# Optimization experiments

Measured on AMD Instinct MI355X. Metric: run time of the kernel, lower is better.

## Reference

```python
import jax, jax.numpy as jnp
import numpy as np

HIDDEN = 256
HORIZON = 24
FMET = 16
OUT = 1
EPS = 1e-5


def setup_inputs() -> dict:
    key = jax.random.key(0)
    ks = jax.random.split(key, 12)
    B, N = 16, 1000
    final_h = jax.random.normal(ks[0], (B, N, HIDDEN), dtype=jnp.float32)
    future_met = jax.random.normal(ks[1], (B, HORIZON, N, FMET), dtype=jnp.float32)
    # step_queries: xavier_uniform over (max_horizon, hidden)
    lim_q = float(np.sqrt(6.0 / (HORIZON + HIDDEN)))
    step_queries = jax.random.uniform(ks[2], (HORIZON, HIDDEN), minval=-lim_q, maxval=lim_q, dtype=jnp.float32)
    # future_met_proj: Linear(FMET -> HIDDEN); store weight as (FMET, HIDDEN)
    lim_fm = float(np.sqrt(1.0 / FMET))
    W_fm = jax.random.uniform(ks[3], (FMET, HIDDEN), minval=-lim_fm, maxval=lim_fm, dtype=jnp.float32)
    b_fm = jax.random.uniform(ks[4], (HIDDEN,), minval=-lim_fm, maxval=lim_fm, dtype=jnp.float32)
    gamma = jnp.ones((HIDDEN,), dtype=jnp.float32)
    beta = jnp.zeros((HIDDEN,), dtype=jnp.float32)
    lim1 = float(np.sqrt(1.0 / HIDDEN))
    W1 = jax.random.uniform(ks[5], (HIDDEN, HIDDEN), minval=-lim1, maxval=lim1, dtype=jnp.float32)
    b1 = jax.random.uniform(ks[6], (HIDDEN,), minval=-lim1, maxval=lim1, dtype=jnp.float32)
    W2 = jax.random.uniform(ks[7], (HIDDEN, OUT), minval=-lim1, maxval=lim1, dtype=jnp.float32)
    b2 = jax.random.uniform(ks[8], (OUT,), minval=-lim1, maxval=lim1, dtype=jnp.float32)
    return {
        "final_h": final_h,
        "future_met": future_met,
        "step_queries": step_queries,
        "W_fm": W_fm,
        "b_fm": b_fm,
        "gamma": gamma,
        "beta": beta,
        "W1": W1,
        "b1": b1,
        "W2": W2,
        "b2": b2,
    }


def _layer_norm(x, gamma, beta):
    mu = jnp.mean(x, axis=-1, keepdims=True)
    var = jnp.mean(jnp.square(x - mu), axis=-1, keepdims=True)
    return (x - mu) * jax.lax.rsqrt(var + EPS) * gamma + beta


def reference(final_h, future_met, step_queries, W_fm, b_fm, gamma, beta, W1, b1, W2, b2):
    # final_h: (B, N, H); future_met: (B, T, N, F)
    # combined: (B, N, T, H) = broadcast(final_h) + queries + proj(future_met)
    combined = final_h[:, :, None, :] + step_queries[None, None, :, :]
    fm = jnp.transpose(future_met, (0, 2, 1, 3))  # (B, N, T, F)
    combined = combined + (jnp.einsum("bntf,fh->bnth", fm, W_fm) + b_fm)
    x = _layer_norm(combined, gamma, beta)
    x = jax.nn.gelu(x @ W1 + b1, approximate=False)
    # dropout is identity in eval mode
    out = x @ W2 + b2  # (B, N, T, OUT)
    return jnp.transpose(out, (0, 2, 1, 3))  # (B, T, N, OUT)
```

## Files before the change

### kernel.cpp

```cpp
#include <hip/hip_runtime.h>
#include <hip/hip_bf16.h>
#include <stdint.h>

#define MROWS 32
#define LDA   264
#define FMS   40

typedef __bf16 bf16x8 __attribute__((ext_vector_type(8)));
typedef float  f32x4  __attribute__((ext_vector_type(4)));
typedef float  f32x2  __attribute__((ext_vector_type(2)));

__device__ __forceinline__ unsigned short f2bf(float f) {
    union { float f; uint32_t u; } v; v.f = f;
    return (unsigned short)((v.u + 0x7FFFu + ((v.u >> 16) & 1u)) >> 16);
}

__device__ __forceinline__ ushort2 pk_bf16(float a, float b) {
    union { __hip_bfloat162 v; ushort2 u; } c;
    c.v = __float22bfloat162_rn(make_float2(a, b));
    return c.u;
}

template <int CTRL>
__device__ __forceinline__ float dpp_radd(float x) {
    union { float f; int i; } a, b;
    a.f = x;
    b.i = __builtin_amdgcn_update_dpp(0, a.i, CTRL, 0xF, 0xF, true);
    return x + b.f;
}
#define ROW_SHR1 0x111
#define ROW_SHR2 0x112
#define ROW_SHR4 0x114
#define ROW_SHR8 0x118
__device__ __forceinline__ float dpp_rowsum(float x) {
    x = dpp_radd<ROW_SHR1>(x);
    x = dpp_radd<ROW_SHR2>(x);
    x = dpp_radd<ROW_SHR4>(x);
    x = dpp_radd<ROW_SHR8>(x);
    return x;
}

__device__ __forceinline__ f32x2 gelu_fast2(f32x2 v) {
    const f32x2 t = v * v;
    f32x2 p = t * 0.044715f + 1.0f;
    const f32x2 u = v * p;
    f32x2 e;
    e.x = __builtin_amdgcn_exp2f(u.x * -2.3021131160186336f);
    e.y = __builtin_amdgcn_exp2f(u.y * -2.3021131160186336f);
    f32x2 r;
    r.x = __builtin_amdgcn_rcpf(1.0f + e.x);
    r.y = __builtin_amdgcn_rcpf(1.0f + e.y);
    return v * r;
}

__device__ __forceinline__ int frag_n(int f) {
    return (f & 0xC0) | ((f & 3) << 4) | ((f >> 2) & 15);
}

__global__ __launch_bounds__(256) void prep1(const float* __restrict__ W1,
                                             const float* __restrict__ step_q,
                                             const float* __restrict__ b_fm,
                                             const float* __restrict__ W_fm,
                                             const float* __restrict__ gamma,
                                             const float* __restrict__ beta,
                                             unsigned short* __restrict__ w1frag,
                                             float* __restrict__ sqb,
                                             unsigned short* __restrict__ wfmfrag,
                                             float* __restrict__ gpart,
                                             float* __restrict__ bpart) {
    const int blk = blockIdx.x, tid = threadIdx.x;
    if (blk < 8) {
        __shared__ unsigned short T[256][40];
        const int kk = blk;
        float sg = 0.f, sb = 0.f;
        #pragma unroll
        for (int r = 0; r < 32; ++r) {
            const int k = (kk << 5) + r;
            const float wv = W1[k * 256 + tid];
            sg = fmaf(gamma[k], wv, sg);
            sb = fmaf(beta[k],  wv, sb);
            T[tid][r] = f2bf(wv);
        }
        gpart[(kk << 8) + tid] = sg;
        bpart[(kk << 8) + tid] = sb;
        __syncthreads();
        #pragma unroll
        for (int f = 0; f < 4; ++f) {
            const int fi = (f << 8) + tid;
            const int l = fi & 63, j = (fi >> 6) & 3, w = fi >> 8;
            const int n = (w << 6) + (j << 4) + (l & 15);
            const uint4 v = *(const uint4*)&T[n][(l >> 4) << 3];
            *(uint4*)&w1frag[((w << 5) + (j << 3) + kk) * 512 + (l << 3)] = v;
        }
    } else if (blk < 32) {
        const int t = blk - 8;
        const int n = frag_n(tid);
        sqb[t * 256 + tid] = step_q[t * 256 + n] + b_fm[n];
    } else {
        const int f  = blk - 32;
        const int fr = (f << 8) + tid;
        const int l = fr & 63, j = (fr >> 6) & 3, w = fr >> 8;
        const int n = (w << 6) + (j << 4) + (l & 15);
        const int qr = l >> 4;
        #pragma unroll
        for (int e = 0; e < 8; ++e) {
            const int k = (qr << 3) + e;
            wfmfrag[(fr << 3) + e] = (k < 16) ? f2bf(W_fm[(k << 8) + n]) : (unsigned short)0;
        }
    }
}

__global__ __launch_bounds__(256) void prep2(const float* __restrict__ gpart,
                                             const float* __restrict__ bpart,
                                             const float* __restrict__ b1,
                                             const float* __restrict__ W2,
                                             const float* __restrict__ gamma,
                                             float* __restrict__ gw1f,
                                             float* __restrict__ b1tf,
                                             float* __restrict__ w2f,
                                             float* __restrict__ gamf) {
    const int tid = threadIdx.x;
    const int n = frag_n(tid);
    float sg = 0.f, sb = 0.f;
    #pragma unroll
    for (int kk = 0; kk < 8; ++kk) {
        sg += gpart[(kk << 8) + n];
        sb += bpart[(kk << 8) + n];
    }
    gw1f[tid] = sg;
    b1tf[tid] = sb + b1[n];
    w2f[tid]  = W2[n];
    gamf[tid] = gamma[n];
}

__global__ __launch_bounds__(256, 6) void fused_head(
    const float* __restrict__ final_h, const float* __restrict__ future_met,
    const float* __restrict__ b2,      const unsigned short* __restrict__ w1frag,
    const float* __restrict__ sqb,     const unsigned short* __restrict__ wfmfrag,
    const float* __restrict__ gw1f,    const float* __restrict__ b1tf,
    const float* __restrict__ w2f,     const float* __restrict__ gamf,
    float* __restrict__ out)
{
    __shared__ __align__(16) unsigned short Abuf[MROWS * LDA];
    __shared__ __align__(16) unsigned short fmA[MROWS * FMS];
    __shared__ float2 red[4][MROWS];
    __shared__ float2 mv[MROWS];
    __shared__ float  part[4][MROWS];

    const int tid = threadIdx.x;
    const int w   = tid >> 6;
    const int l   = tid & 63;
    const int col = l & 15;
    const int qr  = l >> 4;
    const int m0  = blockIdx.x * MROWS;
    const int bn0 = m0 / 24;
    const int tt0 = m0 - bn0 * 24;
    const int fb  = (w << 6) + (col << 2);

    if (tid < 128) {
        const int row = tid >> 2, f0 = (tid & 3) << 2;
        const int tta = tt0 + row;
        const int sub = (tta >= 24) + (tta >= 48);
        const int tt  = tta - sub * 24;
        const int bn  = bn0 + sub;
        const int b   = bn / 1000, n = bn - b * 1000;
        const float4 v = *(const float4*)&future_met[((((b * 24 + tt) * 1000) + n) << 4) + f0];
        ushort2 lo = pk_bf16(v.x, v.y), hi = pk_bf16(v.z, v.w);
        ushort4 o; o.x = lo.x; o.y = lo.y; o.z = hi.x; o.w = hi.y;
        *(ushort4*)&fmA[row * FMS + f0] = o;
    }
    {
        const int row = tid >> 3, k = 16 + ((tid & 7) << 1);
        *(unsigned int*)&fmA[row * FMS + k] = 0u;
    }
    __syncthreads();

    const float4 g4 = *(const float4*)&gamf[fb];
    const f32x2 gA2 = {g4.x, g4.y}, gB2 = {g4.z, g4.w};

    const int dlo = qr << 2;
    const int slo = ((tt0 + dlo) >= 24) + ((tt0 + dlo) >= 48);
    const int shi = ((tt0 + dlo + 19) >= 24) + ((tt0 + dlo + 19) >= 48);
    float flo[4], fhi[4];
    {
        const float* fhl = final_h + ((bn0 + slo) << 8) + (w << 6) + col;
        const float* fhh = final_h + ((bn0 + shi) << 8) + (w << 6) + col;
        #pragma unroll
        for (int j = 0; j < 4; ++j) { flo[j] = fhl[j << 4]; fhi[j] = fhh[j << 4]; }
    }

    f32x4 acc[2][4];
    #pragma unroll
    for (int i = 0; i < 2; ++i) {
        #pragma unroll
        for (int r = 0; r < 4; ++r) {
            const int d   = (i << 4) + (qr << 2) + r;
            const int tta = tt0 + d;
            const int sub = (tta >= 24) + (tta >= 48);
            const int tt  = tta - sub * 24;
            const bool lo = (sub == slo);
            const float4 sb4 = *(const float4*)&sqb[(tt << 8) + fb];
            acc[i][0][r] = (lo ? flo[0] : fhi[0]) + sb4.x;
            acc[i][1][r] = (lo ? flo[1] : fhi[1]) + sb4.y;
            acc[i][2][r] = (lo ? flo[2] : fhi[2]) + sb4.z;
            acc[i][3][r] = (lo ? flo[3] : fhi[3]) + sb4.w;
        }
    }
    {
        const bf16x8 af0 = *(const bf16x8*)&fmA[col * FMS + (qr << 3)];
        const bf16x8 af1 = *(const bf16x8*)&fmA[(16 + col) * FMS + (qr << 3)];
        const unsigned short* Bwf = wfmfrag + (w << 11) + (l << 3);
        #pragma unroll
        for (int j = 0; j < 4; ++j) {
            const bf16x8 bf = *(const bf16x8*)(Bwf + (j << 9));
            acc[0][j] = __builtin_amdgcn_mfma_f32_16x16x32_bf16(af0, bf, acc[0][j], 0, 0, 0);
            acc[1][j] = __builtin_amdgcn_mfma_f32_16x16x32_bf16(af1, bf, acc[1][j], 0, 0, 0);
        }
    }

    #pragma unroll
    for (int i = 0; i < 2; ++i) {
        #pragma unroll
        for (int r = 0; r < 4; ++r) {
            const int m = (i << 4) + (qr << 2) + r;
            const f32x2 vA = {acc[i][0][r], acc[i][1][r]};
            const f32x2 vB = {acc[i][2][r], acc[i][3][r]};
            const f32x2 sv = vA + vB;
            const f32x2 qv = vA * vA + vB * vB;
            float s = sv.x + sv.y;
            float q = qv.x + qv.y;
            const f32x2 vjA = vA * gA2;
            const f32x2 vjB = vB * gB2;
            s = dpp_rowsum(s);
            q = dpp_rowsum(q);
            if (col == 15) red[w][m] = make_float2(s, q);
            const ushort2 p01 = pk_bf16(vjA.x, vjA.y);
            const ushort2 p23 = pk_bf16(vjB.x, vjB.y);
            unsigned short* Ab = &Abuf[m * LDA + (w << 6) + col];
            Ab[0]  = p01.x; Ab[16] = p01.y;
            Ab[32] = p23.x; Ab[48] = p23.y;
        }
    }
    __syncthreads();

    if (tid < MROWS) {
        const float2 a0 = red[0][tid], a1 = red[1][tid], a2 = red[2][tid], a3 = red[3][tid];
        const float S = a0.x + a1.x + a2.x + a3.x;
        const float Q = a0.y + a1.y + a2.y + a3.y;
        const float mu = S * 0.00390625f;
        const float rstd = rsqrtf(Q * 0.00390625f - mu * mu + 1e-5f);
        mv[tid] = make_float2(mu, rstd);
    }

    #pragma unroll
    for (int i = 0; i < 2; ++i)
        #pragma unroll
        for (int j = 0; j < 4; ++j)
            acc[i][j] = (f32x4){0.f, 0.f, 0.f, 0.f};

    {
        const unsigned short* Bw  = w1frag + (w << 14) + (l << 3);
        const unsigned short* Ab0 = &Abuf[col * LDA + (qr << 3)];
        const unsigned short* Ab1 = &Abuf[(16 + col) * LDA + (qr << 3)];
        #pragma unroll
        for (int kk = 0; kk < 8; ++kk) {
            const bf16x8 a0 = *(const bf16x8*)(Ab0 + (kk << 5));
            const bf16x8 a1 = *(const bf16x8*)(Ab1 + (kk << 5));
            #pragma unroll
            for (int j = 0; j < 4; ++j) {
                const bf16x8 bf = *(const bf16x8*)(Bw + (j << 12) + (kk << 9));
                acc[0][j] = __builtin_amdgcn_mfma_f32_16x16x32_bf16(a0, bf, acc[0][j], 0, 0, 0);
                acc[1][j] = __builtin_amdgcn_mfma_f32_16x16x32_bf16(a1, bf, acc[1][j], 0, 0, 0);
            }
        }
    }

    const float4 gw4 = *(const float4*)&gw1f[fb];
    const float4 bt4 = *(const float4*)&b1tf[fb];
    const float4 w24 = *(const float4*)&w2f[fb];
    const f32x2 gwA = {gw4.x, gw4.y}, gwB = {gw4.z, gw4.w};
    const f32x2 btA = {bt4.x, bt4.y}, btB = {bt4.z, bt4.w};
    const f32x2 w2A = {w24.x, w24.y}, w2B = {w24.z, w24.w};
    __syncthreads();

    #pragma unroll
    for (int i = 0; i < 2; ++i) {
        #pragma unroll
        for (int r = 0; r < 4; ++r) {
            const int m = (i << 4) + (qr << 2) + r;
            const float2 p = mv[m];
            const float cm = -p.x * p.y;
            const f32x2 baseA = gwA * cm + btA;
            const f32x2 baseB = gwB * cm + btB;
            const f32x2 accA = {acc[i][0][r], acc[i][1][r]};
            const f32x2 accB = {acc[i][2][r], acc[i][3][r]};
            const f32x2 yA = accA * p.y + baseA;
            const f32x2 yB = accB * p.y + baseB;
            const f32x2 gvA = gelu_fast2(yA);
            const f32x2 gvB = gelu_fast2(yB);
            const f32x2 pp2 = gvA * w2A + gvB * w2B;
            float pp = pp2.x + pp2.y;
            pp = dpp_rowsum(pp);
            if (col == 15) part[w][m] = pp;
        }
    }
    __syncthreads();

    if (tid < MROWS) {
        const int m = m0 + tid;
        const float val = part[0][tid] + part[1][tid] + part[2][tid] + part[3][tid] + b2[0];
        const int bn = m / 24, tt = m - bn * 24;
        const int b  = bn / 1000, n = bn - b * 1000;
        out[(b * 24 + tt) * 1000 + n] = val;
    }
}

extern "C" void kernel_launch(void* const* d_in, const int* in_sizes, int n_in,
                              void* d_out, int out_size, void* d_ws, size_t ws_size,
                              hipStream_t stream) {
    const float* final_h    = (const float*)d_in[0];
    const float* future_met = (const float*)d_in[1];
    const float* step_q     = (const float*)d_in[2];
    const float* W_fm       = (const float*)d_in[3];
    const float* b_fm       = (const float*)d_in[4];
    const float* gamma      = (const float*)d_in[5];
    const float* beta       = (const float*)d_in[6];
    const float* W1         = (const float*)d_in[7];
    const float* b1         = (const float*)d_in[8];
    const float* W2         = (const float*)d_in[9];
    const float* b2         = (const float*)d_in[10];

    unsigned short* w1frag  = (unsigned short*)d_ws;
    float*          sqb     = (float*)((char*)d_ws + 131072);
    unsigned short* wfmfrag = (unsigned short*)((char*)d_ws + 155648);
    float*          gpart   = (float*)((char*)d_ws + 188416);
    float*          bpart   = (float*)((char*)d_ws + 196608);
    float*          gw1f    = (float*)((char*)d_ws + 204800);
    float*          b1tf    = (float*)((char*)d_ws + 205824);
    float*          w2f     = (float*)((char*)d_ws + 206848);
    float*          gamf    = (float*)((char*)d_ws + 207872);
    float* out = (float*)d_out;

    prep1<<<36, 256, 0, stream>>>(W1, step_q, b_fm, W_fm, gamma, beta,
                                  w1frag, sqb, wfmfrag, gpart, bpart);
    prep2<<<1, 256, 0, stream>>>(gpart, bpart, b1, W2, gamma, gw1f, b1tf, w2f, gamf);
    fused_head<<<12000, 256, 0, stream>>>(final_h, future_met, b2,
                                          w1frag, sqb, wfmfrag, gw1f, b1tf, w2f, gamf, out);
}
```

Baseline: 205.1 us.

## Compute LayerNorm stats via MFMA inside GEMM loop, fold gamma into W1

LayerNorm mean and sum of squares are now computed with extra MFMA instructions (A·ones and A·A) inside the W1 GEMM loop instead of DPP row reductions plus a shared-memory cross-wave reduction. Gamma is folded into the bf16 W1 fragments in prep, and A is written to LDS in a permuted column order matched by a frag_n remap of W1's K dimension, allowing vectorized ushort4 stores. One block barrier and the separate stats pass are removed. The cost is extra MFMA work per K step, and the statistics now come from bf16-rounded values, so precision drops slightly.

Measured after the change: 247.4 us. 20.6% more time.

```diff
diff --git a/kernel.cpp b/kernel.cpp
--- a/kernel.cpp
+++ b/kernel.cpp
@@ -75,11 +75,12 @@
         float sg = 0.f, sb = 0.f;
         #pragma unroll
         for (int r = 0; r < 32; ++r) {
-            const int k = (kk << 5) + r;
-            const float wv = W1[k * 256 + tid];
-            sg = fmaf(gamma[k], wv, sg);
-            sb = fmaf(beta[k],  wv, sb);
-            T[tid][r] = f2bf(wv);
+            const int klog = frag_n((kk << 5) + r);
+            const float wv = W1[klog * 256 + tid];
+            const float gv = gamma[klog];
+            sg = fmaf(gv, wv, sg);
+            sb = fmaf(beta[klog], wv, sb);
+            T[tid][r] = f2bf(wv * gv);
         }
         gpart[(kk << 8) + tid] = sg;
         bpart[(kk << 8) + tid] = sb;
@@ -114,11 +115,9 @@
                                              const float* __restrict__ bpart,
                                              const float* __restrict__ b1,
                                              const float* __restrict__ W2,
-                                             const float* __restrict__ gamma,
                                              float* __restrict__ gw1f,
                                              float* __restrict__ b1tf,
-                                             float* __restrict__ w2f,
-                                             float* __restrict__ gamf) {
+                                             float* __restrict__ w2f) {
     const int tid = threadIdx.x;
     const int n = frag_n(tid);
     float sg = 0.f, sb = 0.f;
@@ -130,7 +129,6 @@
     gw1f[tid] = sg;
     b1tf[tid] = sb + b1[n];
     w2f[tid]  = W2[n];
-    gamf[tid] = gamma[n];
 }
 
 __global__ __launch_bounds__(256, 6) void fused_head(
@@ -138,13 +136,11 @@
     const float* __restrict__ b2,      const unsigned short* __restrict__ w1frag,
     const float* __restrict__ sqb,     const unsigned short* __restrict__ wfmfrag,
     const float* __restrict__ gw1f,    const float* __restrict__ b1tf,
-    const float* __restrict__ w2f,     const float* __restrict__ gamf,
-    float* __restrict__ out)
+    const float* __restrict__ w2f,     float* __restrict__ out)
 {
     __shared__ __align__(16) unsigned short Abuf[MROWS * LDA];
     __shared__ __align__(16) unsigned short fmA[MROWS * FMS];
-    __shared__ float2 red[4][MROWS];
-    __shared__ float2 mv[MROWS];
+    __shared__ float2 mvw[4][MROWS];
     __shared__ float  part[4][MROWS];
 
     const int tid = threadIdx.x;
@@ -175,9 +171,6 @@
     }
     __syncthreads();
 
-    const float4 g4 = *(const float4*)&gamf[fb];
-    const f32x2 gA2 = {g4.x, g4.y}, gB2 = {g4.z, g4.w};
-
     const int dlo = qr << 2;
     const int slo = ((tt0 + dlo) >= 24) + ((tt0 + dlo) >= 48);
     const int shi = ((tt0 + dlo + 19) >= 24) + ((tt0 + dlo + 19) >= 48);
@@ -223,40 +216,31 @@
         #pragma unroll
         for (int r = 0; r < 4; ++r) {
             const int m = (i << 4) + (qr << 2) + r;
-            const f32x2 vA = {acc[i][0][r], acc[i][1][r]};
-            const f32x2 vB = {acc[i][2][r], acc[i][3][r]};
-            const f32x2 sv = vA + vB;
-            const f32x2 qv = vA * vA + vB * vB;
-            float s = sv.x + sv.y;
-            float q = qv.x + qv.y;
-            const f32x2 vjA = vA * gA2;
-            const f32x2 vjB = vB * gB2;
-            s = dpp_rowsum(s);
-            q = dpp_rowsum(q);
-            if (col == 15) red[w][m] = make_float2(s, q);
-            const ushort2 p01 = pk_bf16(vjA.x, vjA.y);
-            const ushort2 p23 = pk_bf16(vjB.x, vjB.y);
-            unsigned short* Ab = &Abuf[m * LDA + (w << 6) + col];
-            Ab[0]  = p01.x; Ab[16] = p01.y;
-            Ab[32] = p23.x; Ab[48] = p23.y;
+            const ushort2 p01 = pk_bf16(acc[i][0][r], acc[i][1][r]);
+            const ushort2 p23 = pk_bf16(acc[i][2][r], acc[i][3][r]);
+            ushort4 o; o.x = p01.x; o.y = p01.y; o.z = p23.x; o.w = p23.y;
+            *(ushort4*)&Abuf[m * LDA + (w << 6) + (col << 2)] = o;
         }
     }
     __syncthreads();
-
-    if (tid < MROWS) {
-        const float2 a0 = red[0][tid], a1 = red[1][tid], a2 = red[2][tid], a3 = red[3][tid];
-        const float S = a0.x + a1.x + a2.x + a3.x;
-        const float Q = a0.y + a1.y + a2.y + a3.y;
-        const float mu = S * 0.00390625f;
-        const float rstd = rsqrtf(Q * 0.00390625f - mu * mu + 1e-5f);
-        mv[tid] = make_float2(mu, rstd);
-    }
 
     #pragma unroll
     for (int i = 0; i < 2; ++i)
         #pragma unroll
         for (int j = 0; j < 4; ++j)
             acc[i][j] = (f32x4){0.f, 0.f, 0.f, 0.f};
+    f32x4 accQ[2] = {(f32x4){0.f, 0.f, 0.f, 0.f}, (f32x4){0.f, 0.f, 0.f, 0.f}};
+    f32x4 accS[2] = {(f32x4){0.f, 0.f, 0.f, 0.f}, (f32x4){0.f, 0.f, 0.f, 0.f}};
+    bf16x8 onesf;
+    #pragma unroll
+    for (int e = 0; e < 8; ++e) onesf[e] = (__bf16)1.0f;
+
+    const float4 gw4 = *(const float4*)&gw1f[fb];
+    const float4 bt4 = *(const float4*)&b1tf[fb];
+    const float4 w24 = *(const float4*)&w2f[fb];
+    const f32x2 gwA = {gw4.x, gw4.y}, gwB = {gw4.z, gw4.w};
+    const f32x2 btA = {bt4.x, bt4.y}, btB = {bt4.z, bt4.w};
+    const f32x2 w2A = {w24.x, w24.y}, w2B = {w24.z, w24.w};
 
     {
         const unsigned short* Bw  = w1frag + (w << 14) + (l << 3);
@@ -272,23 +256,31 @@
                 acc[0][j] = __builtin_amdgcn_mfma_f32_16x16x32_bf16(a0, bf, acc[0][j], 0, 0, 0);
                 acc[1][j] = __builtin_amdgcn_mfma_f32_16x16x32_bf16(a1, bf, acc[1][j], 0, 0, 0);
             }
-        }
-    }
-
-    const float4 gw4 = *(const float4*)&gw1f[fb];
-    const float4 bt4 = *(const float4*)&b1tf[fb];
-    const float4 w24 = *(const float4*)&w2f[fb];
-    const f32x2 gwA = {gw4.x, gw4.y}, gwB = {gw4.z, gw4.w};
-    const f32x2 btA = {bt4.x, bt4.y}, btB = {bt4.z, bt4.w};
-    const f32x2 w2A = {w24.x, w24.y}, w2B = {w24.z, w24.w};
-    __syncthreads();
+            accQ[0] = __builtin_amdgcn_mfma_f32_16x16x32_bf16(a0, a0, accQ[0], 0, 0, 0);
+            accQ[1] = __builtin_amdgcn_mfma_f32_16x16x32_bf16(a1, a1, accQ[1], 0, 0, 0);
+            accS[0] = __builtin_amdgcn_mfma_f32_16x16x32_bf16(a0, onesf, accS[0], 0, 0, 0);
+            accS[1] = __builtin_amdgcn_mfma_f32_16x16x32_bf16(a1, onesf, accS[1], 0, 0, 0);
+        }
+    }
+
+    if (qr == (col >> 2)) {
+        #pragma unroll
+        for (int i = 0; i < 2; ++i) {
+            const float S = accS[i][l & 3];
+            const float Q = accQ[i][l & 3];
+            const float mu = S * 0.00390625f;
+            const float rstd = rsqrtf(Q * 0.00390625f - mu * mu + 1e-5f);
+            mvw[w][(i << 4) + col] = make_float2(mu, rstd);
+        }
+    }
+    __threadfence_block();
 
     #pragma unroll
     for (int i = 0; i < 2; ++i) {
         #pragma unroll
         for (int r = 0; r < 4; ++r) {
             const int m = (i << 4) + (qr << 2) + r;
-            const float2 p = mv[m];
+            const float2 p = mvw[w][m];
             const float cm = -p.x * p.y;
             const f32x2 baseA = gwA * cm + btA;
             const f32x2 baseB = gwB * cm + btB;
@@ -338,12 +330,11 @@
     float*          gw1f    = (float*)((char*)d_ws + 204800);
     float*          b1tf    = (float*)((char*)d_ws + 205824);
     float*          w2f     = (float*)((char*)d_ws + 206848);
-    float*          gamf    = (float*)((char*)d_ws + 207872);
     float* out = (float*)d_out;
 
     prep1<<<36, 256, 0, stream>>>(W1, step_q, b_fm, W_fm, gamma, beta,
                                   w1frag, sqb, wfmfrag, gpart, bpart);
-    prep2<<<1, 256, 0, stream>>>(gpart, bpart, b1, W2, gamma, gw1f, b1tf, w2f, gamf);
+    prep2<<<1, 256, 0, stream>>>(gpart, bpart, b1, W2, gw1f, b1tf, w2f);
     fused_head<<<12000, 256, 0, stream>>>(final_h, future_met, b2,
-                                          w1frag, sqb, wfmfrag, gw1f, b1tf, w2f, gamf, out);
-}
+                                          w1frag, sqb, wfmfrag, gw1f, b1tf, w2f, out);
+}
```
